# Kernel tuning notes

Hardware: AMD Instinct MI355X
Metric: run time of the kernel (lower is better)

## Reference

```python
import jax, jax.numpy as jnp
from jax import lax
import numpy as np

B, T_IN, NF, H, T_OUT = 2048, 336, 16, 128, 168


def _gru_cell(x, h, Wih, Whh, bih, bhh):
    # PyTorch GRU cell, gate order [r, z, n]
    gi = x @ Wih.T + bih          # (B, 3H)
    gh = h @ Whh.T + bhh          # (B, 3H)
    i_r, i_z, i_n = jnp.split(gi, 3, axis=-1)
    h_r, h_z, h_n = jnp.split(gh, 3, axis=-1)
    r = jax.nn.sigmoid(i_r + h_r)
    z = jax.nn.sigmoid(i_z + h_z)
    n = jnp.tanh(i_n + r * h_n)
    return (1.0 - z) * n + z * h


def _run_gru_layer(seq_tbf, Wih, Whh, bih, bhh):
    # seq_tbf: (T, B, in_dim) -> (outputs (T,B,H), final hidden (B,H))
    h0 = jnp.zeros((seq_tbf.shape[1], H), seq_tbf.dtype)
    def step(h, xt):
        h2 = _gru_cell(xt, h, Wih, Whh, bih, bhh)
        return h2, h2
    hT, ys = lax.scan(step, h0, seq_tbf)
    return ys, hT


def setup_inputs() -> dict:
    key = jax.random.key(0)
    ks = iter(jax.random.split(key, 32))
    def w(shape, fan):
        return (jax.random.normal(next(ks), shape, jnp.float32) / np.sqrt(fan).astype(np.float32))
    inp = {"x": jax.random.normal(next(ks), (B, T_IN, NF), jnp.float32)}
    inp.update(
        enc_Wih0=w((3 * H, NF), NF), enc_Whh0=w((3 * H, H), H),
        enc_bih0=w((3 * H,), H), enc_bhh0=w((3 * H,), H),
        enc_Wih1=w((3 * H, H), H), enc_Whh1=w((3 * H, H), H),
        enc_bih1=w((3 * H,), H), enc_bhh1=w((3 * H,), H),
        dec_Wih0=w((3 * H, 1), 1), dec_Whh0=w((3 * H, H), H),
        dec_bih0=w((3 * H,), H), dec_bhh0=w((3 * H,), H),
        dec_Wih1=w((3 * H, H), H), dec_Whh1=w((3 * H, H), H),
        dec_bih1=w((3 * H,), H), dec_bhh1=w((3 * H,), H),
        fc_W1=w((H // 2, H), H), fc_b1=w((H // 2,), H),
        fc_W2=w((1, H // 2), H // 2), fc_b2=w((1,), H // 2),
    )
    return inp


def reference(x, enc_Wih0, enc_Whh0, enc_bih0, enc_bhh0,
              enc_Wih1, enc_Whh1, enc_bih1, enc_bhh1,
              dec_Wih0, dec_Whh0, dec_bih0, dec_bhh0,
              dec_Wih1, dec_Whh1, dec_bih1, dec_bhh1,
              fc_W1, fc_b1, fc_W2, fc_b2):
    b = x.shape[0]
    # --- encoder: 2-layer GRU over input sequence (eval mode: dropout off) ---
    seq = jnp.transpose(x, (1, 0, 2))                       # (T_IN, B, NF)
    ys0, h0f = _run_gru_layer(seq, enc_Wih0, enc_Whh0, enc_bih0, enc_bhh0)
    _, h1f = _run_gru_layer(ys0, enc_Wih1, enc_Whh1, enc_bih1, enc_bhh1)

    def dec_step(carry, _):
        h0, h1, inp = carry                                  # inp: (B, 1)
        h0n = _gru_cell(inp, h0, dec_Wih0, dec_Whh0, dec_bih0, dec_bhh0)
        h1n = _gru_cell(h0n, h1, dec_Wih1, dec_Whh1, dec_bih1, dec_bhh1)
        hid = jax.nn.relu(h1n @ fc_W1.T + fc_b1)
        pred = jax.nn.relu(hid @ fc_W2.T + fc_b2)            # (B, 1)
        return (h0n, h1n, pred), pred[:, 0]

    init = (h0f, h1f, jnp.zeros((b, 1), x.dtype))
    _, outs = lax.scan(dec_step, init, None, length=T_OUT)   # (T_OUT, B)
    return outs.T                                            # (B, T_OUT)
```

## Files before the change

kernel.cpp:

```cpp
#include <hip/hip_runtime.h>


typedef unsigned short ushort_t;
typedef unsigned int uint_t;
typedef __attribute__((ext_vector_type(8))) short short8;
typedef __attribute__((ext_vector_type(4))) float f32x4;
typedef __attribute__((ext_vector_type(2))) unsigned int uintx2;

#define BT   8
#define NT   512
#define HD   128
#define TIN  336
#define TOUT 168
#define NFE  16
#define NB   256

#define SC_RZ (-1.44269504089f)
#define SC_N  (-2.88539008177f)

#define OFF_EWHH0 0
#define OFF_EWIH1 6144
#define OFF_EWHH1 12288
#define OFF_DWHH0 18432
#define OFF_DWIH1 24576
#define OFF_DWHH1 30720
#define OFF_EWIH0 36864
#define OFF_FW1   38400

__device__ __forceinline__ ushort_t f2bf(float f) {
    union { float f; uint_t u; } v; v.f = f;
    uint_t r = v.u + 0x7FFFu + ((v.u >> 16) & 1u);
    return (ushort_t)(r >> 16);
}
__device__ __forceinline__ ushort_t f2bf_h(float f) {
    union { float f; uint_t u; } v; v.f = f;
    return (ushort_t)((v.u + 0x8000u) >> 16);
}
__device__ __forceinline__ f32x4 splat4(float v) {
    return (f32x4){v, v, v, v};
}
__device__ __forceinline__ float sig2(float t) {
    return __builtin_amdgcn_rcpf(1.f + __builtin_amdgcn_exp2f(t));
}
__device__ __forceinline__ void barrier_lds() {
    asm volatile("s_waitcnt lgkmcnt(0)\n\ts_barrier" ::: "memory");
}

__device__ __forceinline__ void pl32swap(float& a, float& b) {
    uintx2 r = __builtin_amdgcn_permlane32_swap(
        __float_as_uint(a), __float_as_uint(b), false, false);
    a = __uint_as_float(r[0]);
    b = __uint_as_float(r[1]);
}
__device__ __forceinline__ void spread2(f32x4 v, float& e0, float& e1) {
    float a0 = v[0], a2 = v[2];
    float a1 = v[1], a3 = v[3];
    pl32swap(a0, a2);
    pl32swap(a1, a3);
    e0 = a0; e1 = a1;
}

extern "C" __global__ __launch_bounds__(64)
void prep_kernel(const float* __restrict__ eWhh0, const float* __restrict__ eWih1,
                 const float* __restrict__ eWhh1, const float* __restrict__ dWhh0,
                 const float* __restrict__ dWih1, const float* __restrict__ dWhh1,
                 const float* __restrict__ eWih0, const float* __restrict__ fW1,
                 uint4* __restrict__ ws)
{
    const int g = blockIdx.x;
    const int L = threadIdx.x;
    const int n_lo = L & 15, q = L >> 4;

    const float* src; int n, kb, Ksrc, dst16; float sc;
    if (g < 576) {
        const int m = g / 96, lf = g % 96;
        const float* hs[6] = {eWhh0, eWih1, eWhh1, dWhh0, dWih1, dWhh1};
        src = hs[m];
        const int nt = lf >> 2, kf = lf & 3;
        n = nt * 16 + n_lo; kb = kf * 32 + q * 8; Ksrc = 128;
        dst16 = m * 6144 + lf * 64 + L;
        sc = (n < 2 * HD) ? SC_RZ : SC_N;
    } else if (g < 600) {
        const int nt = g - 576;
        src = eWih0; n = nt * 16 + n_lo; kb = q * 8; Ksrc = 16;
        dst16 = OFF_EWIH0 + nt * 64 + L;
        sc = (n < 2 * HD) ? SC_RZ : SC_N;
    } else {
        const int lf = g - 600;
        src = fW1; n = (lf >> 2) * 16 + n_lo; kb = (lf & 3) * 32 + q * 8; Ksrc = 128;
        dst16 = OFF_FW1 + lf * 64 + L;
        sc = 1.f;
    }

    ushort_t h[8];
    #pragma unroll
    for (int j = 0; j < 8; ++j) {
        const int k = kb + j;
        h[j] = (k < Ksrc) ? f2bf(sc * src[n * Ksrc + k]) : (ushort_t)0;
    }
    uint4 o;
    o.x = (uint_t)h[0] | ((uint_t)h[1] << 16);
    o.y = (uint_t)h[2] | ((uint_t)h[3] << 16);
    o.z = (uint_t)h[4] | ((uint_t)h[5] << 16);
    o.w = (uint_t)h[6] | ((uint_t)h[7] << 16);
    ws[dst16] = o;
}

__device__ __forceinline__ void combineS(const f32x4& gr, const f32x4& gz,
                                         const f32x4& gn_i, const f32x4& gn_h,
                                         float* hreg, ushort_t* wb)
{
    float r_[2], z_[2], i_[2], n_[2];
    spread2(gr,   r_[0], r_[1]);
    spread2(gz,   z_[0], z_[1]);
    spread2(gn_i, i_[0], i_[1]);
    spread2(gn_h, n_[0], n_[1]);
    #pragma unroll
    for (int e = 0; e < 2; ++e) {
        const float rg = sig2(r_[e]);
        const float zg = sig2(z_[e]);
        const float ng = fmaf(2.f, sig2(i_[e] + rg * n_[e]), -1.f);
        const float hn = fmaf(zg, hreg[e] - ng, ng);
        hreg[e] = hn;
        wb[e * 8] = f2bf_h(hn);
    }
}

extern "C" __global__ __launch_bounds__(NT, 2)
void gru_seq2seq_kernel(
    const float* __restrict__ x,
    const float* __restrict__ ebih0, const float* __restrict__ ebhh0,
    const float* __restrict__ ebih1, const float* __restrict__ ebhh1,
    const float* __restrict__ dWih0, const float* __restrict__ dbih0,
    const float* __restrict__ dbhh0,
    const float* __restrict__ dbih1, const float* __restrict__ dbhh1,
    const float* __restrict__ fb1, const float* __restrict__ fW2,
    const float* __restrict__ fb2,
    const short8* __restrict__ wf,
    float* __restrict__ out)
{
    __shared__ ushort_t h0f[2][4][512];
    __shared__ ushort_t h1f[2][4][512];
    __shared__ ushort_t xf[2][512];
    __shared__ uint4 fw1l[1024];

    const int t = threadIdx.x;
    const int L = t & 63, w = t >> 6;
    const int col16 = L & 15, q = L >> 4;
    const int col = w * 16 + col16;
    const int b0 = blockIdx.x * BT;

    for (int i = t; i < 4096; i += NT) {
        (&h0f[0][0][0])[i] = 0;
        (&h1f[0][0][0])[i] = 0;
    }
    for (int i = t; i < 1024; i += NT) (&xf[0][0])[i] = 0;

    const int kfc = col >> 5, qq = (col >> 3) & 3, jc = col & 7;
    const int hi2 = (L >> 5) * 2;
    const int hwoE = kfc * 512 + (qq * 16 + (q & 1) * 4 + hi2) * 8 + jc;

    const int xr = t >> 4, xfeat = t & 15;
    const int xscat = (((xfeat >> 3) * 16) + (xr & 15)) * 8 + (xfeat & 7);
    float xv = (t < 128) ? x[((b0 + xr) * TIN + 0) * NFE + xfeat] : 0.f;

    const float e0_rz = SC_RZ * (ebih0[col] + ebhh0[col]);
    const float e0_zz = SC_RZ * (ebih0[HD + col] + ebhh0[HD + col]);
    const float e0_in = SC_N * ebih0[2 * HD + col];
    const float e0_hn = SC_N * ebhh0[2 * HD + col];
    const float e1_rz = SC_RZ * (ebih1[col] + ebhh1[col]);
    const float e1_zz = SC_RZ * (ebih1[HD + col] + ebhh1[HD + col]);
    const float e1_in = SC_N * ebih1[2 * HD + col];
    const float e1_hn = SC_N * ebhh1[2 * HD + col];

    float h0r[2] = {0, 0};
    float h1r[2] = {0, 0};

    short8 Wa[3][4], Wb[3][4], Wc[3][4];
    short8 We[3];
    #pragma unroll
    for (int t3 = 0; t3 < 3; ++t3) {
        const int nt = w + t3 * 8;
        We[t3] = wf[OFF_EWIH0 + nt * 64 + L];
        #pragma unroll
        for (int kf = 0; kf < 4; ++kf) {
            Wa[t3][kf] = wf[OFF_EWHH0 + (nt * 4 + kf) * 64 + L];
            Wb[t3][kf] = wf[OFF_EWIH1 + (nt * 4 + kf) * 64 + L];
            Wc[t3][kf] = wf[OFF_EWHH1 + (nt * 4 + kf) * 64 + L];
        }
    }

    barrier_lds();
    if (t < 128) {
        (&xf[0][0])[xscat] = f2bf_h(xv);
        xv = x[((b0 + xr) * TIN + 1) * NFE + xfeat];
    }
    barrier_lds();

    {
        if (t < 128) {
            (&xf[0][0])[512 + xscat] = f2bf_h(xv);
            xv = x[((b0 + xr) * TIN + 2) * NFE + xfeat];
        }
        const short8 Ax = *(const short8*)&xf[0][L * 8];
        short8 Ah[4];
        #pragma unroll
        for (int kf = 0; kf < 4; ++kf)
            Ah[kf] = *(const short8*)&h0f[0][kf][L * 8];
        f32x4 gr = splat4(e0_rz), gz = splat4(e0_zz);
        f32x4 gni = splat4(e0_in), gnh = splat4(e0_hn);
        #pragma unroll
        for (int kf = 0; kf < 4; ++kf) {
            gr  = __builtin_amdgcn_mfma_f32_16x16x32_bf16(Ah[kf], Wa[0][kf], gr,  0, 0, 0);
            gz  = __builtin_amdgcn_mfma_f32_16x16x32_bf16(Ah[kf], Wa[1][kf], gz,  0, 0, 0);
            gnh = __builtin_amdgcn_mfma_f32_16x16x32_bf16(Ah[kf], Wa[2][kf], gnh, 0, 0, 0);
        }
        gr  = __builtin_amdgcn_mfma_f32_16x16x32_bf16(Ax, We[0], gr,  0, 0, 0);
        gz  = __builtin_amdgcn_mfma_f32_16x16x32_bf16(Ax, We[1], gz,  0, 0, 0);
        gni = __builtin_amdgcn_mfma_f32_16x16x32_bf16(Ax, We[2], gni, 0, 0, 0);
        combineS(gr, gz, gni, gnh, h0r, &(&h0f[0][0][0])[2048 + hwoE]);
        barrier_lds();
    }

    for (int i = 1; i < TIN; ++i) {
        const int p = i & 1;
        if (t < 128 && i + 1 < TIN) {
            (&xf[0][0])[(1 - p) * 512 + xscat] = f2bf_h(xv);
            if (i + 2 < TIN) xv = x[((b0 + xr) * TIN + i + 2) * NFE + xfeat];
        }
        const short8 Ax = *(const short8*)&xf[p][L * 8];
        short8 Ah0[4], Ah1[4];
        #pragma unroll
        for (int kf = 0; kf < 4; ++kf) {
            Ah0[kf] = *(const short8*)&h0f[p][kf][L * 8];
            Ah1[kf] = *(const short8*)&h1f[p][kf][L * 8];
        }
        f32x4 a_r = splat4(e0_rz), a_z = splat4(e0_zz);
        f32x4 a_ni = splat4(e0_in), a_nh = splat4(e0_hn);
        f32x4 b_r = splat4(e1_rz), b_z = splat4(e1_zz);
        f32x4 b_ni = splat4(e1_in), b_nh = splat4(e1_hn);
        #pragma unroll
        for (int kf = 0; kf < 4; ++kf) {
            a_r  = __builtin_amdgcn_mfma_f32_16x16x32_bf16(Ah0[kf], Wa[0][kf], a_r,  0, 0, 0);
            a_z  = __builtin_amdgcn_mfma_f32_16x16x32_bf16(Ah0[kf], Wa[1][kf], a_z,  0, 0, 0);
            a_nh = __builtin_amdgcn_mfma_f32_16x16x32_bf16(Ah0[kf], Wa[2][kf], a_nh, 0, 0, 0);
            b_r  = __builtin_amdgcn_mfma_f32_16x16x32_bf16(Ah0[kf], Wb[0][kf], b_r,  0, 0, 0);
            b_z  = __builtin_amdgcn_mfma_f32_16x16x32_bf16(Ah0[kf], Wb[1][kf], b_z,  0, 0, 0);
            b_ni = __builtin_amdgcn_mfma_f32_16x16x32_bf16(Ah0[kf], Wb[2][kf], b_ni, 0, 0, 0);
            b_r  = __builtin_amdgcn_mfma_f32_16x16x32_bf16(Ah1[kf], Wc[0][kf], b_r,  0, 0, 0);
            b_z  = __builtin_amdgcn_mfma_f32_16x16x32_bf16(Ah1[kf], Wc[1][kf], b_z,  0, 0, 0);
            b_nh = __builtin_amdgcn_mfma_f32_16x16x32_bf16(Ah1[kf], Wc[2][kf], b_nh, 0, 0, 0);
        }
        a_r  = __builtin_amdgcn_mfma_f32_16x16x32_bf16(Ax, We[0], a_r,  0, 0, 0);
        a_z  = __builtin_amdgcn_mfma_f32_16x16x32_bf16(Ax, We[1], a_z,  0, 0, 0);
        a_ni = __builtin_amdgcn_mfma_f32_16x16x32_bf16(Ax, We[2], a_ni, 0, 0, 0);

        combineS(a_r, a_z, a_ni, a_nh, h0r, &(&h0f[0][0][0])[(1 - p) * 2048 + hwoE]);
        combineS(b_r, b_z, b_ni, b_nh, h1r, &(&h1f[0][0][0])[(1 - p) * 2048 + hwoE]);
        barrier_lds();
    }

    {
        short8 Ai[4], Ah[4];
        #pragma unroll
        for (int kf = 0; kf < 4; ++kf) {
            Ai[kf] = *(const short8*)&h0f[0][kf][L * 8];
            Ah[kf] = *(const short8*)&h1f[0][kf][L * 8];
        }
        f32x4 gr = splat4(e1_rz), gz = splat4(e1_zz);
        f32x4 gni = splat4(e1_in), gnh = splat4(e1_hn);
        #pragma unroll
        for (int kf = 0; kf < 4; ++kf) {
            gr  = __builtin_amdgcn_mfma_f32_16x16x32_bf16(Ai[kf], Wb[0][kf], gr,  0, 0, 0);
            gz  = __builtin_amdgcn_mfma_f32_16x16x32_bf16(Ai[kf], Wb[1][kf], gz,  0, 0, 0);
            gni = __builtin_amdgcn_mfma_f32_16x16x32_bf16(Ai[kf], Wb[2][kf], gni, 0, 0, 0);
            gr  = __builtin_amdgcn_mfma_f32_16x16x32_bf16(Ah[kf], Wc[0][kf], gr,  0, 0, 0);
            gz  = __builtin_amdgcn_mfma_f32_16x16x32_bf16(Ah[kf], Wc[1][kf], gz,  0, 0, 0);
            gnh = __builtin_amdgcn_mfma_f32_16x16x32_bf16(Ah[kf], Wc[2][kf], gnh, 0, 0, 0);
        }
        combineS(gr, gz, gni, gnh, h1r, &(&h1f[0][0][0])[2048 + hwoE]);
        barrier_lds();
    }

    asm volatile("" ::: "memory");

    #pragma unroll
    for (int t3 = 0; t3 < 3; ++t3) {
        const int nt = w + t3 * 8;
        #pragma unroll
        for (int kf = 0; kf < 4; ++kf) {
            Wa[t3][kf] = wf[OFF_DWHH0 + (nt * 4 + kf) * 64 + L];
            Wb[t3][kf] = wf[OFF_DWIH1 + (nt * 4 + kf) * 64 + L];
            Wc[t3][kf] = wf[OFF_DWHH1 + (nt * 4 + kf) * 64 + L];
        }
    }
    for (int i = t; i < 1024; i += NT) fw1l[i] = ((const uint4*)wf)[OFF_FW1 + i];

    const float d0_rz = SC_RZ * (dbih0[col] + dbhh0[col]);
    const float d0_zz = SC_RZ * (dbih0[HD + col] + dbhh0[HD + col]);
    const float d0_in = SC_N * dbih0[2 * HD + col];
    const float d0_hn = SC_N * dbhh0[2 * HD + col];
    const float d1_rz = SC_RZ * (dbih1[col] + dbhh1[col]);
    const float d1_zz = SC_RZ * (dbih1[HD + col] + dbhh1[HD + col]);
    const float d1_in = SC_N * dbih1[2 * HD + col];
    const float d1_hn = SC_N * dbhh1[2 * HD + col];
    const float w0r = SC_RZ * dWih0[col];
    const float w0z = SC_RZ * dWih0[HD + col];
    const float w0n = SC_N * dWih0[2 * HD + col];
    float f1bv[4], w2v[4];
    #pragma unroll
    for (int nt = 0; nt < 4; ++nt) {
        f1bv[nt] = fb1[nt * 16 + col16];
        w2v[nt]  = fW2[nt * 16 + col16];
    }
    const float fb2v = fb2[0];
    float ivr[2] = {0.f, 0.f};

    {
        short8 Ah[4];
        #pragma unroll
        for (int kf = 0; kf < 4; ++kf)
            Ah[kf] = *(const short8*)&h0f[0][kf][L * 8];
        f32x4 g0 = splat4(d0_rz), g1 = splat4(d0_zz), g2 = splat4(d0_hn);
        #pragma unroll
        for (int kf = 0; kf < 4; ++kf) {
            g0 = __builtin_amdgcn_mfma_f32_16x16x32_bf16(Ah[kf], Wa[0][kf], g0, 0, 0, 0);
            g1 = __builtin_amdgcn_mfma_f32_16x16x32_bf16(Ah[kf], Wa[1][kf], g1, 0, 0, 0);
            g2 = __builtin_amdgcn_mfma_f32_16x16x32_bf16(Ah[kf], Wa[2][kf], g2, 0, 0, 0);
        }
        float g0e[2], g1e[2], g2e[2];
        spread2(g0, g0e[0], g0e[1]);
        spread2(g1, g1e[0], g1e[1]);
        spread2(g2, g2e[0], g2e[1]);
        barrier_lds();
        ushort_t* wb = &(&h0f[0][0][0])[0 + hwoE];
        #pragma unroll
        for (int e = 0; e < 2; ++e) {
            const float rg = sig2(g0e[e]);
            const float zg = sig2(g1e[e]);
            const float ng = fmaf(2.f, sig2(d0_in + rg * g2e[e]), -1.f);
            const float hn = fmaf(zg, h0r[e] - ng, ng);
            h0r[e] = hn;
            wb[e * 8] = f2bf_h(hn);
        }
    }
    barrier_lds();

    for (int s = 0; s < TOUT; ++s) {
        const int p = s & 1;

        {
            short8 Ai[4], Ah[4];
            #pragma unroll
            for (int kf = 0; kf < 4; ++kf) {
                Ai[kf] = *(const short8*)&h0f[p][kf][L * 8];
                Ah[kf] = *(const short8*)&h1f[1 - p][kf][L * 8];
            }
            f32x4 gr = splat4(d1_rz), gz = splat4(d1_zz);
            f32x4 gni = splat4(d1_in), gnh = splat4(d1_hn);
            #pragma unroll
            for (int kf = 0; kf < 4; ++kf) {
                gr  = __builtin_amdgcn_mfma_f32_16x16x32_bf16(Ai[kf], Wb[0][kf], gr,  0, 0, 0);
                gz  = __builtin_amdgcn_mfma_f32_16x16x32_bf16(Ai[kf], Wb[1][kf], gz,  0, 0, 0);
                gni = __builtin_amdgcn_mfma_f32_16x16x32_bf16(Ai[kf], Wb[2][kf], gni, 0, 0, 0);
                gr  = __builtin_amdgcn_mfma_f32_16x16x32_bf16(Ah[kf], Wc[0][kf], gr,  0, 0, 0);
                gz  = __builtin_amdgcn_mfma_f32_16x16x32_bf16(Ah[kf], Wc[1][kf], gz,  0, 0, 0);
                gnh = __builtin_amdgcn_mfma_f32_16x16x32_bf16(Ah[kf], Wc[2][kf], gnh, 0, 0, 0);
            }
            combineS(gr, gz, gni, gnh, h1r, &(&h1f[0][0][0])[p * 2048 + hwoE]);
        }
        barrier_lds();

        {
            short8 Af[4], Ah[4];
            #pragma unroll
            for (int kf = 0; kf < 4; ++kf) {
                Af[kf] = *(const short8*)&h1f[p][kf][L * 8];
                Ah[kf] = *(const short8*)&h0f[p][kf][L * 8];
            }
            f32x4 g0 = splat4(d0_rz), g1 = splat4(d0_zz), g2 = splat4(d0_hn);
            f32x4 fc[4];
            #pragma unroll
            for (int nt = 0; nt < 4; ++nt) fc[nt] = splat4(0.f);
            #pragma unroll
            for (int kf = 0; kf < 4; ++kf) {
                g0 = __builtin_amdgcn_mfma_f32_16x16x32_bf16(Ah[kf], Wa[0][kf], g0, 0, 0, 0);
                g1 = __builtin_amdgcn_mfma_f32_16x16x32_bf16(Ah[kf], Wa[1][kf], g1, 0, 0, 0);
                g2 = __builtin_amdgcn_mfma_f32_16x16x32_bf16(Ah[kf], Wa[2][kf], g2, 0, 0, 0);
                #pragma unroll
                for (int nt = 0; nt < 4; ++nt) {
                    const short8 b = *(const short8*)&fw1l[(nt * 4 + kf) * 64 + L];
                    fc[nt] = __builtin_amdgcn_mfma_f32_16x16x32_bf16(Af[kf], b, fc[nt], 0, 0, 0);
                }
            }
            float g0e[2], g1e[2], g2e[2], fe0[4], fe1[4];
            spread2(g0, g0e[0], g0e[1]);
            spread2(g1, g1e[0], g1e[1]);
            spread2(g2, g2e[0], g2e[1]);
            #pragma unroll
            for (int nt = 0; nt < 4; ++nt) spread2(fc[nt], fe0[nt], fe1[nt]);
            float ps[2];
            #pragma unroll
            for (int e = 0; e < 2; ++e) {
                float s_ = 0.f;
                #pragma unroll
                for (int nt = 0; nt < 4; ++nt) {
                    const float v = (e == 0) ? fe0[nt] : fe1[nt];
                    s_ = fmaf(fmaxf(v + f1bv[nt], 0.f), w2v[nt], s_);
                }
                ps[e] = s_;
            }
            #pragma unroll
            for (int e = 0; e < 2; ++e) {
                ps[e] += __shfl_xor(ps[e], 1, 64);
                ps[e] += __shfl_xor(ps[e], 2, 64);
                ps[e] += __shfl_xor(ps[e], 4, 64);
                ps[e] += __shfl_xor(ps[e], 8, 64);
                ivr[e] = fmaxf(ps[e] + fb2v, 0.f);
            }
            if (w == 0 && col16 == 0) {
                #pragma unroll
                for (int e = 0; e < 2; ++e)
                    out[(b0 + (q & 1) * 4 + hi2 + e) * TOUT + s] = ivr[e];
            }
            ushort_t* wb = &(&h0f[0][0][0])[(1 - p) * 2048 + hwoE];
            #pragma unroll
            for (int e = 0; e < 2; ++e) {
                const float iv = ivr[e];
                const float rg = sig2(fmaf(iv, w0r, g0e[e]));
                const float zg = sig2(fmaf(iv, w0z, g1e[e]));
                const float tt = fmaf(iv, w0n, d0_in) + rg * g2e[e];
                const float ng = fmaf(2.f, sig2(tt), -1.f);
                const float hn = fmaf(zg, h0r[e] - ng, ng);
                h0r[e] = hn;
                wb[e * 8] = f2bf_h(hn);
            }
        }
        barrier_lds();
    }
}

extern "C" void kernel_launch(void* const* d_in, const int* in_sizes, int n_in,
                              void* d_out, int out_size, void* d_ws, size_t ws_size,
                              hipStream_t stream) {
    const float* x     = (const float*)d_in[0];
    const float* eWih0 = (const float*)d_in[1];
    const float* eWhh0 = (const float*)d_in[2];
    const float* ebih0 = (const float*)d_in[3];
    const float* ebhh0 = (const float*)d_in[4];
    const float* eWih1 = (const float*)d_in[5];
    const float* eWhh1 = (const float*)d_in[6];
    const float* ebih1 = (const float*)d_in[7];
    const float* ebhh1 = (const float*)d_in[8];
    const float* dWih0 = (const float*)d_in[9];
    const float* dWhh0 = (const float*)d_in[10];
    const float* dbih0 = (const float*)d_in[11];
    const float* dbhh0 = (const float*)d_in[12];
    const float* dWih1 = (const float*)d_in[13];
    const float* dWhh1 = (const float*)d_in[14];
    const float* dbih1 = (const float*)d_in[15];
    const float* dbhh1 = (const float*)d_in[16];
    const float* fW1   = (const float*)d_in[17];
    const float* fb1   = (const float*)d_in[18];
    const float* fW2   = (const float*)d_in[19];
    const float* fb2   = (const float*)d_in[20];
    float* out = (float*)d_out;

    hipLaunchKernelGGL(prep_kernel, dim3(616), dim3(64), 0, stream,
                       eWhh0, eWih1, eWhh1, dWhh0, dWih1, dWhh1, eWih0, fW1,
                       (uint4*)d_ws);
    hipLaunchKernelGGL(gru_seq2seq_kernel, dim3(NB), dim3(NT), 0, stream,
                       x, ebih0, ebhh0, ebih1, ebhh1,
                       dWih0, dbih0, dbhh0, dbih1, dbhh1,
                       fb1, fW2, fb2,
                       (const short8*)d_ws, out);
}
```

Measured before the change: 740.9 us.

## Stagger MFMA/VALU phases across waves, raise MFMA priority, use DPP reductions

Half of the waves now run the layer-1 (B) MFMA chain before the layer-0 (A) chain, and the other half the reverse. In the decoder, half the waves run the FC MFMAs before the gate MFMAs. The aim is for one group's gate math (VALU) to overlap another group's matrix work instead of all waves contending for the same unit at once. MFMA blocks are wrapped in s_setprio(1) so waves issuing matrix instructions get scheduling priority. The 16-lane butterfly reduction of the FC output switches from __shfl_xor to DPP quad_perm/row_ror adds, which shortens the serial decoder critical path. The risks are higher register pressure from holding both accumulator sets live and uncertain benefit from priority hints.

```diff
diff --git a/kernel.cpp b/kernel.cpp
--- a/kernel.cpp
+++ b/kernel.cpp
@@ -58,6 +58,19 @@
     pl32swap(a0, a2);
     pl32swap(a1, a3);
     e0 = a0; e1 = a1;
+}
+
+template <int CTRL>
+__device__ __forceinline__ float dpp_add(float acc) {
+    int x = __builtin_amdgcn_update_dpp(0, __float_as_int(acc), CTRL, 0xF, 0xF, true);
+    return acc + __int_as_float(x);
+}
+__device__ __forceinline__ float sum16(float v) {
+    v = dpp_add<0xB1>(v);
+    v = dpp_add<0x4E>(v);
+    v = dpp_add<0x124>(v);
+    v = dpp_add<0x128>(v);
+    return v;
 }
 
 extern "C" __global__ __launch_bounds__(64)
@@ -149,6 +162,7 @@
     const int col16 = L & 15, q = L >> 4;
     const int col = w * 16 + col16;
     const int b0 = blockIdx.x * BT;
+    const bool wlo = (w < 4);
 
     for (int i = t; i < 4096; i += NT) {
         (&h0f[0][0][0])[i] = 0;
@@ -209,6 +223,7 @@
             Ah[kf] = *(const short8*)&h0f[0][kf][L * 8];
         f32x4 gr = splat4(e0_rz), gz = splat4(e0_zz);
         f32x4 gni = splat4(e0_in), gnh = splat4(e0_hn);
+        __builtin_amdgcn_s_setprio(1);
         #pragma unroll
         for (int kf = 0; kf < 4; ++kf) {
             gr  = __builtin_amdgcn_mfma_f32_16x16x32_bf16(Ah[kf], Wa[0][kf], gr,  0, 0, 0);
@@ -218,6 +233,7 @@
         gr  = __builtin_amdgcn_mfma_f32_16x16x32_bf16(Ax, We[0], gr,  0, 0, 0);
         gz  = __builtin_amdgcn_mfma_f32_16x16x32_bf16(Ax, We[1], gz,  0, 0, 0);
         gni = __builtin_amdgcn_mfma_f32_16x16x32_bf16(Ax, We[2], gni, 0, 0, 0);
+        __builtin_amdgcn_s_setprio(0);
         combineS(gr, gz, gni, gnh, h0r, &(&h0f[0][0][0])[2048 + hwoE]);
         barrier_lds();
     }
@@ -235,28 +251,48 @@
             Ah0[kf] = *(const short8*)&h0f[p][kf][L * 8];
             Ah1[kf] = *(const short8*)&h1f[p][kf][L * 8];
         }
-        f32x4 a_r = splat4(e0_rz), a_z = splat4(e0_zz);
-        f32x4 a_ni = splat4(e0_in), a_nh = splat4(e0_hn);
-        f32x4 b_r = splat4(e1_rz), b_z = splat4(e1_zz);
-        f32x4 b_ni = splat4(e1_in), b_nh = splat4(e1_hn);
-        #pragma unroll
-        for (int kf = 0; kf < 4; ++kf) {
-            a_r  = __builtin_amdgcn_mfma_f32_16x16x32_bf16(Ah0[kf], Wa[0][kf], a_r,  0, 0, 0);
-            a_z  = __builtin_amdgcn_mfma_f32_16x16x32_bf16(Ah0[kf], Wa[1][kf], a_z,  0, 0, 0);
-            a_nh = __builtin_amdgcn_mfma_f32_16x16x32_bf16(Ah0[kf], Wa[2][kf], a_nh, 0, 0, 0);
-            b_r  = __builtin_amdgcn_mfma_f32_16x16x32_bf16(Ah0[kf], Wb[0][kf], b_r,  0, 0, 0);
-            b_z  = __builtin_amdgcn_mfma_f32_16x16x32_bf16(Ah0[kf], Wb[1][kf], b_z,  0, 0, 0);
-            b_ni = __builtin_amdgcn_mfma_f32_16x16x32_bf16(Ah0[kf], Wb[2][kf], b_ni, 0, 0, 0);
-            b_r  = __builtin_amdgcn_mfma_f32_16x16x32_bf16(Ah1[kf], Wc[0][kf], b_r,  0, 0, 0);
-            b_z  = __builtin_amdgcn_mfma_f32_16x16x32_bf16(Ah1[kf], Wc[1][kf], b_z,  0, 0, 0);
-            b_nh = __builtin_amdgcn_mfma_f32_16x16x32_bf16(Ah1[kf], Wc[2][kf], b_nh, 0, 0, 0);
-        }
-        a_r  = __builtin_amdgcn_mfma_f32_16x16x32_bf16(Ax, We[0], a_r,  0, 0, 0);
-        a_z  = __builtin_amdgcn_mfma_f32_16x16x32_bf16(Ax, We[1], a_z,  0, 0, 0);
-        a_ni = __builtin_amdgcn_mfma_f32_16x16x32_bf16(Ax, We[2], a_ni, 0, 0, 0);
-
-        combineS(a_r, a_z, a_ni, a_nh, h0r, &(&h0f[0][0][0])[(1 - p) * 2048 + hwoE]);
-        combineS(b_r, b_z, b_ni, b_nh, h1r, &(&h1f[0][0][0])[(1 - p) * 2048 + hwoE]);
+        f32x4 a_r, a_z, a_ni, a_nh;
+        f32x4 b_r, b_z, b_ni, b_nh;
+
+        auto doA = [&]() {
+            a_r = splat4(e0_rz); a_z = splat4(e0_zz);
+            a_ni = splat4(e0_in); a_nh = splat4(e0_hn);
+            __builtin_amdgcn_s_setprio(1);
+            #pragma unroll
+            for (int kf = 0; kf < 4; ++kf) {
+                a_r  = __builtin_amdgcn_mfma_f32_16x16x32_bf16(Ah0[kf], Wa[0][kf], a_r,  0, 0, 0);
+                a_z  = __builtin_amdgcn_mfma_f32_16x16x32_bf16(Ah0[kf], Wa[1][kf], a_z,  0, 0, 0);
+                a_nh = __builtin_amdgcn_mfma_f32_16x16x32_bf16(Ah0[kf], Wa[2][kf], a_nh, 0, 0, 0);
+            }
+            a_r  = __builtin_amdgcn_mfma_f32_16x16x32_bf16(Ax, We[0], a_r,  0, 0, 0);
+            a_z  = __builtin_amdgcn_mfma_f32_16x16x32_bf16(Ax, We[1], a_z,  0, 0, 0);
+            a_ni = __builtin_amdgcn_mfma_f32_16x16x32_bf16(Ax, We[2], a_ni, 0, 0, 0);
+            __builtin_amdgcn_s_setprio(0);
+        };
+        auto doB = [&]() {
+            b_r = splat4(e1_rz); b_z = splat4(e1_zz);
+            b_ni = splat4(e1_in); b_nh = splat4(e1_hn);
+            __builtin_amdgcn_s_setprio(1);
+            #pragma unroll
+            for (int kf = 0; kf < 4; ++kf) {
+                b_r  = __builtin_amdgcn_mfma_f32_16x16x32_bf16(Ah0[kf], Wb[0][kf], b_r,  0, 0, 0);
+                b_z  = __builtin_amdgcn_mfma_f32_16x16x32_bf16(Ah0[kf], Wb[1][kf], b_z,  0, 0, 0);
+                b_ni = __builtin_amdgcn_mfma_f32_16x16x32_bf16(Ah0[kf], Wb[2][kf], b_ni, 0, 0, 0);
+                b_r  = __builtin_amdgcn_mfma_f32_16x16x32_bf16(Ah1[kf], Wc[0][kf], b_r,  0, 0, 0);
+                b_z  = __builtin_amdgcn_mfma_f32_16x16x32_bf16(Ah1[kf], Wc[1][kf], b_z,  0, 0, 0);
+                b_nh = __builtin_amdgcn_mfma_f32_16x16x32_bf16(Ah1[kf], Wc[2][kf], b_nh, 0, 0, 0);
+            }
+            __builtin_amdgcn_s_setprio(0);
+        };
+        auto doCA = [&]() {
+            combineS(a_r, a_z, a_ni, a_nh, h0r, &(&h0f[0][0][0])[(1 - p) * 2048 + hwoE]);
+        };
+        auto doCB = [&]() {
+            combineS(b_r, b_z, b_ni, b_nh, h1r, &(&h1f[0][0][0])[(1 - p) * 2048 + hwoE]);
+        };
+
+        if (wlo) { doA(); doB(); doCA(); doCB(); }
+        else     { doB(); doA(); doCB(); doCA(); }
         barrier_lds();
     }
 
@@ -269,6 +305,7 @@
         }
         f32x4 gr = splat4(e1_rz), gz = splat4(e1_zz);
         f32x4 gni = splat4(e1_in), gnh = splat4(e1_hn);
+        __builtin_amdgcn_s_setprio(1);
         #pragma unroll
         for (int kf = 0; kf < 4; ++kf) {
             gr  = __builtin_amdgcn_mfma_f32_16x16x32_bf16(Ai[kf], Wb[0][kf], gr,  0, 0, 0);
@@ -278,6 +315,7 @@
             gz  = __builtin_amdgcn_mfma_f32_16x16x32_bf16(Ah[kf], Wc[1][kf], gz,  0, 0, 0);
             gnh = __builtin_amdgcn_mfma_f32_16x16x32_bf16(Ah[kf], Wc[2][kf], gnh, 0, 0, 0);
         }
+        __builtin_amdgcn_s_setprio(0);
         combineS(gr, gz, gni, gnh, h1r, &(&h1f[0][0][0])[2048 + hwoE]);
         barrier_lds();
     }
@@ -322,12 +360,14 @@
         for (int kf = 0; kf < 4; ++kf)
             Ah[kf] = *(const short8*)&h0f[0][kf][L * 8];
         f32x4 g0 = splat4(d0_rz), g1 = splat4(d0_zz), g2 = splat4(d0_hn);
+        __builtin_amdgcn_s_setprio(1);
         #pragma unroll
         for (int kf = 0; kf < 4; ++kf) {
             g0 = __builtin_amdgcn_mfma_f32_16x16x32_bf16(Ah[kf], Wa[0][kf], g0, 0, 0, 0);
             g1 = __builtin_amdgcn_mfma_f32_16x16x32_bf16(Ah[kf], Wa[1][kf], g1, 0, 0, 0);
             g2 = __builtin_amdgcn_mfma_f32_16x16x32_bf16(Ah[kf], Wa[2][kf], g2, 0, 0, 0);
         }
+        __builtin_amdgcn_s_setprio(0);
         float g0e[2], g1e[2], g2e[2];
         spread2(g0, g0e[0], g0e[1]);
         spread2(g1, g1e[0], g1e[1]);
@@ -358,6 +398,7 @@
             }
             f32x4 gr = splat4(d1_rz), gz = splat4(d1_zz);
             f32x4 gni = splat4(d1_in), gnh = splat4(d1_hn);
+            __builtin_amdgcn_s_setprio(1);
             #pragma unroll
             for (int kf = 0; kf < 4; ++kf) {
                 gr  = __builtin_amdgcn_mfma_f32_16x16x32_bf16(Ai[kf], Wb[0][kf], gr,  0, 0, 0);
@@ -367,6 +408,7 @@
                 gz  = __builtin_amdgcn_mfma_f32_16x16x32_bf16(Ah[kf], Wc[1][kf], gz,  0, 0, 0);
                 gnh = __builtin_amdgcn_mfma_f32_16x16x32_bf16(Ah[kf], Wc[2][kf], gnh, 0, 0, 0);
             }
+            __builtin_amdgcn_s_setprio(0);
             combineS(gr, gz, gni, gnh, h1r, &(&h1f[0][0][0])[p * 2048 + hwoE]);
         }
         barrier_lds();
@@ -378,25 +420,38 @@
                 Af[kf] = *(const short8*)&h1f[p][kf][L * 8];
                 Ah[kf] = *(const short8*)&h0f[p][kf][L * 8];
             }
-            f32x4 g0 = splat4(d0_rz), g1 = splat4(d0_zz), g2 = splat4(d0_hn);
+            f32x4 g0, g1, g2;
             f32x4 fc[4];
-            #pragma unroll
-            for (int nt = 0; nt < 4; ++nt) fc[nt] = splat4(0.f);
-            #pragma unroll
-            for (int kf = 0; kf < 4; ++kf) {
-                g0 = __builtin_amdgcn_mfma_f32_16x16x32_bf16(Ah[kf], Wa[0][kf], g0, 0, 0, 0);
-                g1 = __builtin_amdgcn_mfma_f32_16x16x32_bf16(Ah[kf], Wa[1][kf], g1, 0, 0, 0);
-                g2 = __builtin_amdgcn_mfma_f32_16x16x32_bf16(Ah[kf], Wa[2][kf], g2, 0, 0, 0);
+
+            auto doG = [&]() {
+                g0 = splat4(d0_rz); g1 = splat4(d0_zz); g2 = splat4(d0_hn);
+                __builtin_amdgcn_s_setprio(1);
                 #pragma unroll
-                for (int nt = 0; nt < 4; ++nt) {
-                    const short8 b = *(const short8*)&fw1l[(nt * 4 + kf) * 64 + L];
-                    fc[nt] = __builtin_amdgcn_mfma_f32_16x16x32_bf16(Af[kf], b, fc[nt], 0, 0, 0);
+                for (int kf = 0; kf < 4; ++kf) {
+                    g0 = __builtin_amdgcn_mfma_f32_16x16x32_bf16(Ah[kf], Wa[0][kf], g0, 0, 0, 0);
+                    g1 = __builtin_amdgcn_mfma_f32_16x16x32_bf16(Ah[kf], Wa[1][kf], g1, 0, 0, 0);
+                    g2 = __builtin_amdgcn_mfma_f32_16x16x32_bf16(Ah[kf], Wa[2][kf], g2, 0, 0, 0);
                 }
-            }
+                __builtin_amdgcn_s_setprio(0);
+            };
+            auto doF = [&]() {
+                #pragma unroll
+                for (int nt = 0; nt < 4; ++nt) fc[nt] = splat4(0.f);
+                __builtin_amdgcn_s_setprio(1);
+                #pragma unroll
+                for (int kf = 0; kf < 4; ++kf) {
+                    #pragma unroll
+                    for (int nt = 0; nt < 4; ++nt) {
+                        const short8 b = *(const short8*)&fw1l[(nt * 4 + kf) * 64 + L];
+                        fc[nt] = __builtin_amdgcn_mfma_f32_16x16x32_bf16(Af[kf], b, fc[nt], 0, 0, 0);
+                    }
+                }
+                __builtin_amdgcn_s_setprio(0);
+            };
+            if (wlo) { doG(); doF(); }
+            else     { doF(); doG(); }
+
             float g0e[2], g1e[2], g2e[2], fe0[4], fe1[4];
-            spread2(g0, g0e[0], g0e[1]);
-            spread2(g1, g1e[0], g1e[1]);
-            spread2(g2, g2e[0], g2e[1]);
             #pragma unroll
             for (int nt = 0; nt < 4; ++nt) spread2(fc[nt], fe0[nt], fe1[nt]);
             float ps[2];
@@ -412,12 +467,12 @@
             }
             #pragma unroll
             for (int e = 0; e < 2; ++e) {
-                ps[e] += __shfl_xor(ps[e], 1, 64);
-                ps[e] += __shfl_xor(ps[e], 2, 64);
-                ps[e] += __shfl_xor(ps[e], 4, 64);
-                ps[e] += __shfl_xor(ps[e], 8, 64);
+                ps[e] = sum16(ps[e]);
                 ivr[e] = fmaxf(ps[e] + fb2v, 0.f);
             }
+            spread2(g0, g0e[0], g0e[1]);
+            spread2(g1, g1e[0], g1e[1]);
+            spread2(g2, g2e[0], g2e[1]);
             if (w == 0 && col16 == 0) {
                 #pragma unroll
                 for (int e = 0; e < 2; ++e)
```

Result: slower. 837.8 us (+13.1%).
